# Kernel tuning notes

Measured on AMD Instinct MI355X. Metric: run time of the kernel, lower is better.

The kernel has to match this reference:

```python
import jax, jax.numpy as jnp
import numpy as np
from jax import lax

EPS = 1e-20
_A, _B, _C = slice(None, -2), slice(1, -1), slice(2, None)
# 4 direction pairs: (up-left, down-right), (up, down), (up-right, down-left), (right, left)
_OFFS = [((_A, _A), (_C, _C)), ((_A, _B), (_C, _B)), ((_A, _C), (_C, _A)), ((_B, _C), (_B, _A))]


def _neigh(x, pad_val):
    # x: [B,C,H,W] -> [B,C,9,H,W] of 3x3 neighborhoods (stride 1, pad 1)
    B, C, H, W = x.shape
    xp = jnp.pad(x, ((0, 0), (0, 0), (1, 1), (1, 1)), constant_values=pad_val)
    return jnp.stack([xp[:, :, i:i + H, j:j + W] for i in range(3) for j in range(3)], axis=2)


def _take(n, j):
    return jnp.take_along_axis(n, j, axis=2)[:, :, 0]


def _pair_stack(lo, hi, op):
    # -> [B,C,2,4,H,W]; mirrors the torch stack-of-stacks over 4 directions x 2 orderings
    return jnp.stack([jnp.stack([op(lo[:, :, r1, c1], hi[:, :, r2, c2]),
                                 op(hi[:, :, r1, c1], lo[:, :, r2, c2])], axis=2)
                      for (r1, c1), (r2, c2) in _OFFS], axis=3)


def _forward(d, cd, e, ce, w_prop, w_s_from_d, channel_weight, spatial_weight):
    B, C, H, W = d.shape
    O4 = spatial_weight.shape[0]
    O = O4 // 4
    # pad like F.pad(d, (1,1,1,1))
    dp = jnp.pad(d, ((0, 0), (0, 0), (1, 1), (1, 1)))
    cdp = jnp.pad(cd, ((0, 0), (0, 0), (1, 1), (1, 1)))
    # max_pool2d(k=3,s=1,p=1, return_indices) equivalent: argmax over 3x3 neighborhood,
    # then gather d / cd at those indices (retrieve_indices)
    j_max = jnp.argmax(_neigh(dp * cdp, -np.inf), axis=2, keepdims=True)
    j_min = jnp.argmax(_neigh(cdp / (dp + EPS), -np.inf), axis=2, keepdims=True)
    nd, ncd = _neigh(dp, 0.0), _neigh(cdp, 0.0)
    d_min, d_max = _take(nd, j_min), _take(nd, j_max)
    cd_min, cd_max = _take(ncd, j_min), _take(ncd, j_max)
    # directional depth ratios and confidence products: [B,C,2,4,H,W]
    d_ratio = jnp.clip(_pair_stack(d_min, d_max, lambda a, b: a / (b + EPS)), EPS, 1.0) ** w_s_from_d
    c_ratio = _pair_stack(cd_min, cd_max, lambda a, b: a * b)
    j = jnp.argmax(c_ratio / d_ratio, axis=2, keepdims=True)
    e_from_d = _take(d_ratio, j)   # [B,C,4,H,W]
    ce_from_d = _take(c_ratio, j)  # [B,C,4,H,W]
    # confidence-weighted propagation, then flatten to [B, C*4, H, W]
    e = ((w_prop * ce * e + ce_from_d * e_from_d) / (w_prop * ce + ce_from_d + EPS)).reshape(B, C * 4, H, W)
    ce = ((w_prop * ce + ce_from_d) / (w_prop + 1.0)).reshape(B, C * 4, H, W)
    # 1x1 channel mixing conv (groups=1)
    cw = channel_weight[:, :, 0, 0]  # [O*4, C*4]
    nom = jnp.einsum('bihw,oi->bohw', ce * e, cw)
    den = jnp.einsum('bihw,oi->bohw', ce, cw)
    e = nom / (den + EPS)
    ce = den / (jnp.sum(channel_weight) + EPS)
    # depthwise spatial conv (groups = out*4), stride=1, padding=k//2
    K = spatial_weight.shape[-1]
    p = K // 2
    dw = lambda x: lax.conv_general_dilated(x, spatial_weight, (1, 1), ((p, p), (p, p)),
                                            feature_group_count=O4,
                                            dimension_numbers=('NCHW', 'OIHW', 'NCHW'))
    nom = dw(ce * e).reshape(B, O, 4, H, W)
    den = dw(ce).reshape(B, O, 4, H, W)
    return nom / (den + EPS), den / (jnp.sum(spatial_weight) + EPS)


def setup_inputs() -> dict:
    key = jax.random.key(0)
    ks = jax.random.split(key, 8)
    B, C, O, H, W, K = 4, 32, 32, 192, 192, 5
    d = jax.random.uniform(ks[0], (B, C, H, W), jnp.float32)
    cd = jax.random.uniform(ks[1], (B, C, H, W), jnp.float32)
    e = jax.random.uniform(ks[2], (B, C, 4, H, W), jnp.float32)
    ce = jax.random.uniform(ks[3], (B, C, 4, H, W), jnp.float32)
    # parameters; positive as enforced by enforce_limits() (softplus) in the original
    w_prop = jax.random.uniform(ks[4], (1, C, 1, 1, 1), jnp.float32, 0.5, 1.5)
    w_s_from_d = jax.random.uniform(ks[5], (1, C, 2, 4, 1, 1), jnp.float32, 0.5, 2.0)
    channel_weight = jax.random.uniform(ks[6], (O * 4, C * 4, 1, 1), jnp.float32)
    spatial_weight = jax.random.uniform(ks[7], (O * 4, 1, K, K), jnp.float32)
    return dict(d=d, cd=cd, e=e, ce=ce, w_prop=w_prop, w_s_from_d=w_s_from_d,
                channel_weight=channel_weight, spatial_weight=spatial_weight)


def reference(d, cd, e, ce, w_prop, w_s_from_d, channel_weight, spatial_weight):
    return _forward(d, cd, e, ce, w_prop, w_s_from_d, channel_weight, spatial_weight)
```

## Files before the change

kernel.cpp:

```cpp
#include <hip/hip_runtime.h>
#include <stdint.h>

#define EPS 1e-20f
#define H_ 192
#define W_ 192
#define HW_ 36864
#define CH4 128
#define OUTELEMS 18874368

typedef __attribute__((ext_vector_type(8))) short bf16x8;
typedef __attribute__((ext_vector_type(4))) float f32x4;

__device__ __forceinline__ unsigned short f2bf(float f) {
  unsigned u = __float_as_uint(f);
  return (unsigned short)((u + 0x7fffu + ((u >> 16) & 1u)) >> 16);
}
__device__ __forceinline__ float bflo(unsigned v) { return __uint_as_float(v << 16); }
__device__ __forceinline__ float bfhi(unsigned v) { return __uint_as_float(v & 0xffff0000u); }

__global__ void __launch_bounds__(256) k0_prep(const float* __restrict__ cw,
                                               const float* __restrict__ sw,
                                               unsigned short* __restrict__ AWhi,
                                               unsigned short* __restrict__ AWlo,
                                               float* __restrict__ sums) {
  int tid = threadIdx.x;
  if (blockIdx.x < 64) {
    int n = blockIdx.x * 256 + tid;
    int t = n & 7;
    int l = (n >> 3) & 63;
    int kb = (n >> 9) & 3;
    int ot = n >> 11;
    int o = ot * 16 + (l & 15);
    int i = kb * 32 + (l >> 4) * 8 + t;
    float wv = cw[o * 128 + i];
    unsigned short hi = f2bf(wv);
    float hif = bflo((unsigned)hi);
    unsigned short lo = f2bf(wv - hif);
    AWhi[n] = hi;
    AWlo[n] = lo;
  } else {
    __shared__ float red[256];
    float s = 0.f;
    for (int k = tid; k < 16384; k += 256) s += cw[k];
    red[tid] = s; __syncthreads();
    for (int off = 128; off > 0; off >>= 1) {
      if (tid < off) red[tid] += red[tid + off];
      __syncthreads();
    }
    if (tid == 0) sums[0] = red[0];
    __syncthreads();
    s = 0.f;
    for (int k = tid; k < 3200; k += 256) s += sw[k];
    red[tid] = s; __syncthreads();
    for (int off = 128; off > 0; off >>= 1) {
      if (tid < off) red[tid] += red[tid + off];
      __syncthreads();
    }
    if (tid == 0) sums[1] = red[0];
  }
}

__global__ void __launch_bounds__(256) k1_stage1(
    const float* __restrict__ d, const float* __restrict__ cd,
    const float* __restrict__ e, const float* __restrict__ ce,
    const float* __restrict__ wprop, const float* __restrict__ wsd,
    unsigned* __restrict__ XY) {
  const int tid = threadIdx.x;
  const int tile = blockIdx.x;
  const int th0 = (tile / 6) * 32, tw0 = (tile % 6) * 32;
  const int bc = blockIdx.y;
  const int b = bc >> 5, c = bc & 31;

  __shared__ float S[5184];
  float* dpL = S;
  float* cdpL = S + 1296;
  float* kxL = S + 2592;
  float* knL = S + 3888;

  const float* dB = d + bc * HW_;
  const float* cdB = cd + bc * HW_;
  for (int idx = tid; idx < 1296; idx += 256) {
    int ly = idx / 36, lx = idx % 36;
    int gy = th0 + ly - 2, gx = tw0 + lx - 2;
    float dv = 0.f, cv = 0.f;
    if (gy >= 0 && gy < H_ && gx >= 0 && gx < W_) {
      dv = dB[gy * W_ + gx];
      cv = cdB[gy * W_ + gx];
    }
    dpL[idx] = dv; cdpL[idx] = cv;
    bool inb = (gy >= -1) & (gy <= H_) & (gx >= -1) & (gx <= W_);
    kxL[idx] = inb ? dv * cv : -1.f;
    knL[idx] = inb ? cv / (dv + EPS) : -1.f;
  }
  __syncthreads();

  float rdmn[5], rdmx[5], rcmn[5], rcmx[5];
#pragma unroll
  for (int i = 0; i < 5; ++i) {
    int idx = i * 256 + tid;
    if (idx < 1156) {
      int ly = idx / 34, lx = idx % 34;
      int base = ly * 36 + lx;
      float bkx = -1.f, bkn = -1.f;
      int ox = base + 37, on = base + 37;
#pragma unroll
      for (int di = 0; di < 3; ++di) {
#pragma unroll
        for (int dj = 0; dj < 3; ++dj) {
          int o = base + di * 36 + dj;
          float kx = kxL[o], kn = knL[o];
          if (kx > bkx) { bkx = kx; ox = o; }
          if (kn > bkn) { bkn = kn; on = o; }
        }
      }
      rdmx[i] = dpL[ox]; rcmx[i] = cdpL[ox];
      rdmn[i] = dpL[on]; rcmn[i] = cdpL[on];
    } else {
      rdmx[i] = 0.f; rcmx[i] = 0.f; rdmn[i] = 0.f; rcmn[i] = 0.f;
    }
  }
  __syncthreads();

  float* DMN = S;
  float* DMX = S + 1190;
  float* CMN = S + 2380;
  float* CMX = S + 3570;
#pragma unroll
  for (int i = 0; i < 5; ++i) {
    int idx = i * 256 + tid;
    if (idx < 1156) {
      int ly = idx / 34, lx = idx % 34;
      int m = ly * 35 + lx;
      DMN[m] = rdmn[i]; DMX[m] = rdmx[i];
      CMN[m] = rcmn[i]; CMX[m] = rcmx[i];
    }
  }
  __syncthreads();

  const float wp = wprop[c];
  const float iwp1 = __builtin_amdgcn_rcpf(wp + 1.0f);
  float wq[8];
#pragma unroll
  for (int t = 0; t < 8; ++t) wq[t] = wsd[c * 8 + t];

  const int offy[4] = {-1, -1, -1, 0};
  const int offx[4] = {-1, 0, 1, 1};

  const int ly = tid >> 3, lx4 = (tid & 7) << 2;
  const int hh = th0 + ly, ww0 = tw0 + lx4;
#pragma unroll
  for (int p = 0; p < 4; ++p) {
    int n1 = (ly + offy[p] + 1) * 35 + (lx4 + offx[p] + 1);
    int n2 = (ly - offy[p] + 1) * 35 + (lx4 - offx[p] + 1);
    int ei = (bc * 4 + p) * HW_ + hh * W_ + ww0;
    float4 ev4 = *reinterpret_cast<const float4*>(&e[ei]);
    float4 cev4 = *reinterpret_cast<const float4*>(&ce[ei]);
    const float* evp = &ev4.x;
    const float* cevp = &cev4.x;
    unsigned ow[4];
#pragma unroll
    for (int k = 0; k < 4; ++k) {
      float dmn1 = DMN[n1 + k], cmn1 = CMN[n1 + k];
      float dmx1 = DMX[n1 + k], cmx1 = CMX[n1 + k];
      float dmn2 = DMN[n2 + k], cmn2 = CMN[n2 + k];
      float dmx2 = DMX[n2 + k], cmx2 = CMX[n2 + k];
      float r0 = dmn1 * __builtin_amdgcn_rcpf(dmx2 + EPS);
      float r1 = dmx1 * __builtin_amdgcn_rcpf(dmn2 + EPS);
      float cr0 = cmn1 * cmx2;
      float cr1 = cmx1 * cmn2;
      float x0 = fminf(fmaxf(r0, EPS), 1.0f);
      float x1 = fminf(fmaxf(r1, EPS), 1.0f);
      float dr0 = __builtin_amdgcn_exp2f(wq[p] * __builtin_amdgcn_logf(x0));
      float dr1 = __builtin_amdgcn_exp2f(wq[4 + p] * __builtin_amdgcn_logf(x1));
      float ef, cf;
      if (cr1 * dr0 > cr0 * dr1) { ef = dr1; cf = cr1; } else { ef = dr0; cf = cr0; }
      float ev = evp[k], cev = cevp[k];
      float dn = wp * cev + cf;
      float e1 = (wp * cev * ev + cf * ef) * __builtin_amdgcn_rcpf(dn + EPS);
      float ce1 = dn * iwp1;
      ow[k] = (unsigned)f2bf(ce1 * e1) | ((unsigned)f2bf(ce1) << 16);
    }
    unsigned* xo = &XY[(b * CH4 + c * 4 + p) * HW_ + hh * W_ + ww0];
    *reinterpret_cast<uint4*>(xo) = make_uint4(ow[0], ow[1], ow[2], ow[3]);
  }
}

__global__ void __launch_bounds__(256) k2_mix(const unsigned* __restrict__ XY,
                                              const unsigned short* __restrict__ AWhi,
                                              const unsigned short* __restrict__ AWlo,
                                              const float* __restrict__ sums,
                                              unsigned* __restrict__ PQ) {
  __shared__ unsigned L[128 * 66];
  const int tid = threadIdx.x;
  const int blk = blockIdx.x;
  const int b = blk / 576;
  const int hw0 = (blk % 576) * 64;
  const unsigned* xp = XY + (size_t)(b * CH4) * HW_ + hw0;

#pragma unroll
  for (int j = 0; j < 8; ++j) {
    int v = j * 256 + tid;
    int ch = v >> 4;
    int po = (v & 15) * 4;
    uint4 val = *reinterpret_cast<const uint4*>(xp + (size_t)ch * HW_ + po);
    unsigned* dst = &L[ch * 66 + po];
    *reinterpret_cast<uint2*>(dst) = make_uint2(val.x, val.y);
    *reinterpret_cast<uint2*>(dst + 2) = make_uint2(val.z, val.w);
  }
  __syncthreads();

  const int lane = tid & 63;
  const int w = tid >> 6;
  const int c = lane & 15;
  const int g = lane >> 4;
  const int pbase = w * 16 + c;

  bf16x8 xf[4], yf[4];
#pragma unroll
  for (int kb = 0; kb < 4; ++kb) {
    unsigned vv[8];
    const unsigned* base = &L[(kb * 32 + g * 8) * 66 + pbase];
#pragma unroll
    for (int t = 0; t < 8; ++t) vv[t] = base[t * 66];
    union { bf16x8 v; unsigned u[4]; } ux, uy;
#pragma unroll
    for (int p = 0; p < 4; ++p) {
      ux.u[p] = (vv[2 * p] & 0xffffu) | (vv[2 * p + 1] << 16);
      uy.u[p] = (vv[2 * p] >> 16) | (vv[2 * p + 1] & 0xffff0000u);
    }
    xf[kb] = ux.v;
    yf[kb] = uy.v;
  }

  const float inv = 1.0f / (sums[0] + EPS);
  unsigned* qp = PQ + (size_t)(b * CH4) * HW_ + hw0;

#pragma unroll 2
  for (int ot = 0; ot < 8; ++ot) {
    f32x4 accn = {0.f, 0.f, 0.f, 0.f};
    f32x4 accd = {0.f, 0.f, 0.f, 0.f};
#pragma unroll
    for (int kb = 0; kb < 4; ++kb) {
      int an = ((ot * 4 + kb) * 64 + lane) * 8;
      bf16x8 ahi = *reinterpret_cast<const bf16x8*>(AWhi + an);
      bf16x8 alo = *reinterpret_cast<const bf16x8*>(AWlo + an);
      accn = __builtin_amdgcn_mfma_f32_16x16x32_bf16(ahi, xf[kb], accn, 0, 0, 0);
      accn = __builtin_amdgcn_mfma_f32_16x16x32_bf16(alo, xf[kb], accn, 0, 0, 0);
      accd = __builtin_amdgcn_mfma_f32_16x16x32_bf16(ahi, yf[kb], accd, 0, 0, 0);
      accd = __builtin_amdgcn_mfma_f32_16x16x32_bf16(alo, yf[kb], accd, 0, 0, 0);
    }
#pragma unroll
    for (int j = 0; j < 4; ++j) {
      int o = ot * 16 + g * 4 + j;
      qp[(size_t)o * HW_ + w * 16 + c] =
          (unsigned)f2bf(accn[j] * inv) | ((unsigned)f2bf(accd[j] * inv) << 16);
    }
  }
}

__global__ void __launch_bounds__(256) k3_conv(const unsigned* __restrict__ PQ,
                                               const float* __restrict__ sw,
                                               const float* __restrict__ sums,
                                               float* __restrict__ out0,
                                               float* __restrict__ out1) {
  int t = blockIdx.x;
  int tile = t % 36;
  int chb = t / 36;
  int ch = chb & 127;
  int th0 = (tile / 6) * 32, tw0 = (tile % 6) * 32;
  __shared__ float Pt[1296], Qt[1296];
  const unsigned* src = PQ + chb * HW_;
  int tid = threadIdx.x;
  for (int idx = tid; idx < 1296; idx += 256) {
    int ly = idx / 36, lx = idx % 36;
    int gy = th0 + ly - 2, gx = tw0 + lx - 2;
    unsigned v = 0;
    if (gy >= 0 && gy < H_ && gx >= 0 && gx < W_) v = src[gy * W_ + gx];
    Pt[idx] = bflo(v); Qt[idx] = bfhi(v);
  }
  __syncthreads();
  float wr[25];
#pragma unroll
  for (int k = 0; k < 25; ++k) wr[k] = sw[ch * 25 + k];
  float isw = 1.0f / (sums[1] + EPS);
  int x = tid & 31, yg = tid >> 5;
  float an[4] = {0, 0, 0, 0}, ad[4] = {0, 0, 0, 0};
#pragma unroll
  for (int rr = 0; rr < 8; ++rr) {
    int Lr = yg * 4 + rr;
    float pv[5], qv[5];
#pragma unroll
    for (int c5 = 0; c5 < 5; ++c5) {
      pv[c5] = Pt[Lr * 36 + x + c5];
      qv[c5] = Qt[Lr * 36 + x + c5];
    }
#pragma unroll
    for (int k = 0; k < 4; ++k) {
      int ky = rr - k;
      if (ky >= 0 && ky <= 4) {
#pragma unroll
        for (int c5 = 0; c5 < 5; ++c5) {
          an[k] += pv[c5] * wr[ky * 5 + c5];
          ad[k] += qv[c5] * wr[ky * 5 + c5];
        }
      }
    }
  }
#pragma unroll
  for (int k = 0; k < 4; ++k) {
    int hh = th0 + yg * 4 + k;
    int oi = chb * HW_ + hh * W_ + tw0 + x;
    out0[oi] = an[k] / (ad[k] + EPS);
    out1[oi] = ad[k] * isw;
  }
}

extern "C" void kernel_launch(void* const* d_in, const int* in_sizes, int n_in,
                              void* d_out, int out_size, void* d_ws, size_t ws_size,
                              hipStream_t stream) {
  const float* d = (const float*)d_in[0];
  const float* cd = (const float*)d_in[1];
  const float* e = (const float*)d_in[2];
  const float* ce = (const float*)d_in[3];
  const float* wprop = (const float*)d_in[4];
  const float* wsd = (const float*)d_in[5];
  const float* cw = (const float*)d_in[6];
  const float* sw = (const float*)d_in[7];

  float* wsf = (float*)d_ws;
  float* sums = wsf;
  unsigned short* AWhi = (unsigned short*)(wsf + 64);
  unsigned short* AWlo = AWhi + 16384;
  unsigned* PQ = (unsigned*)(wsf + 64 + 16384);
  float* out0 = (float*)d_out;
  float* out1 = out0 + OUTELEMS;
  unsigned* XY = (unsigned*)(out0 + OUTELEMS);

  hipLaunchKernelGGL(k0_prep, dim3(65), dim3(256), 0, stream, cw, sw, AWhi, AWlo, sums);
  hipLaunchKernelGGL(k1_stage1, dim3(36, 128), dim3(256), 0, stream, d, cd, e, ce,
                     wprop, wsd, XY);
  hipLaunchKernelGGL(k2_mix, dim3(2304), dim3(256), 0, stream, XY, AWhi, AWlo, sums, PQ);
  hipLaunchKernelGGL(k3_conv, dim3(18432), dim3(256), 0, stream, PQ, sw, sums, out0,
                     out1);
}
```

Baseline: 417.5 us.

## Vectorize LDS/global loads across stages and drop LDS staging in mix kernel

```diff
diff --git a/kernel.cpp b/kernel.cpp
--- a/kernel.cpp
+++ b/kernel.cpp
@@ -71,11 +71,10 @@
   const int bc = blockIdx.y;
   const int b = bc >> 5, c = bc & 31;
 
-  __shared__ float S[5184];
-  float* dpL = S;
-  float* cdpL = S + 1296;
-  float* kxL = S + 2592;
-  float* knL = S + 3888;
+  __shared__ float2 S2[2592];
+  float2* K2 = S2;
+  float2* V2 = S2 + 1296;
+  float* S = (float*)S2;
 
   const float* dB = d + bc * HW_;
   const float* cdB = cd + bc * HW_;
@@ -87,10 +86,11 @@
       dv = dB[gy * W_ + gx];
       cv = cdB[gy * W_ + gx];
     }
-    dpL[idx] = dv; cdpL[idx] = cv;
     bool inb = (gy >= -1) & (gy <= H_) & (gx >= -1) & (gx <= W_);
-    kxL[idx] = inb ? dv * cv : -1.f;
-    knL[idx] = inb ? cv / (dv + EPS) : -1.f;
+    float kx = inb ? dv * cv : -1.f;
+    float kn = inb ? cv / (dv + EPS) : -1.f;
+    K2[idx] = make_float2(kx, kn);
+    V2[idx] = make_float2(dv, cv);
   }
   __syncthreads();
 
@@ -108,13 +108,14 @@
 #pragma unroll
         for (int dj = 0; dj < 3; ++dj) {
           int o = base + di * 36 + dj;
-          float kx = kxL[o], kn = knL[o];
-          if (kx > bkx) { bkx = kx; ox = o; }
-          if (kn > bkn) { bkn = kn; on = o; }
+          float2 kk = K2[o];
+          if (kk.x > bkx) { bkx = kk.x; ox = o; }
+          if (kk.y > bkn) { bkn = kk.y; on = o; }
         }
       }
-      rdmx[i] = dpL[ox]; rcmx[i] = cdpL[ox];
-      rdmn[i] = dpL[on]; rcmn[i] = cdpL[on];
+      float2 vx = V2[ox], vn = V2[on];
+      rdmx[i] = vx.x; rcmx[i] = vx.y;
+      rdmn[i] = vn.x; rcmn[i] = vn.y;
     } else {
       rdmx[i] = 0.f; rcmx[i] = 0.f; rdmn[i] = 0.f; rcmn[i] = 0.f;
     }
@@ -148,15 +149,19 @@
 
   const int ly = tid >> 3, lx4 = (tid & 7) << 2;
   const int hh = th0 + ly, ww0 = tw0 + lx4;
+  float4 ev4[4], cev4[4];
+#pragma unroll
+  for (int p = 0; p < 4; ++p) {
+    int ei = (bc * 4 + p) * HW_ + hh * W_ + ww0;
+    ev4[p] = *reinterpret_cast<const float4*>(&e[ei]);
+    cev4[p] = *reinterpret_cast<const float4*>(&ce[ei]);
+  }
 #pragma unroll
   for (int p = 0; p < 4; ++p) {
     int n1 = (ly + offy[p] + 1) * 35 + (lx4 + offx[p] + 1);
     int n2 = (ly - offy[p] + 1) * 35 + (lx4 - offx[p] + 1);
-    int ei = (bc * 4 + p) * HW_ + hh * W_ + ww0;
-    float4 ev4 = *reinterpret_cast<const float4*>(&e[ei]);
-    float4 cev4 = *reinterpret_cast<const float4*>(&ce[ei]);
-    const float* evp = &ev4.x;
-    const float* cevp = &cev4.x;
+    const float* evp = &ev4[p].x;
+    const float* cevp = &cev4[p].x;
     unsigned ow[4];
 #pragma unroll
     for (int k = 0; k < 4; ++k) {
@@ -190,38 +195,24 @@
                                               const unsigned short* __restrict__ AWlo,
                                               const float* __restrict__ sums,
                                               unsigned* __restrict__ PQ) {
-  __shared__ unsigned L[128 * 66];
   const int tid = threadIdx.x;
   const int blk = blockIdx.x;
   const int b = blk / 576;
   const int hw0 = (blk % 576) * 64;
-  const unsigned* xp = XY + (size_t)(b * CH4) * HW_ + hw0;
-
-#pragma unroll
-  for (int j = 0; j < 8; ++j) {
-    int v = j * 256 + tid;
-    int ch = v >> 4;
-    int po = (v & 15) * 4;
-    uint4 val = *reinterpret_cast<const uint4*>(xp + (size_t)ch * HW_ + po);
-    unsigned* dst = &L[ch * 66 + po];
-    *reinterpret_cast<uint2*>(dst) = make_uint2(val.x, val.y);
-    *reinterpret_cast<uint2*>(dst + 2) = make_uint2(val.z, val.w);
-  }
-  __syncthreads();
 
   const int lane = tid & 63;
   const int w = tid >> 6;
   const int c = lane & 15;
   const int g = lane >> 4;
-  const int pbase = w * 16 + c;
+  const int px = hw0 + w * 16 + c;
+  const unsigned* xp = XY + (size_t)(b * CH4) * HW_ + px;
 
   bf16x8 xf[4], yf[4];
 #pragma unroll
   for (int kb = 0; kb < 4; ++kb) {
     unsigned vv[8];
-    const unsigned* base = &L[(kb * 32 + g * 8) * 66 + pbase];
-#pragma unroll
-    for (int t = 0; t < 8; ++t) vv[t] = base[t * 66];
+#pragma unroll
+    for (int t = 0; t < 8; ++t) vv[t] = xp[(size_t)(kb * 32 + g * 8 + t) * HW_];
     union { bf16x8 v; unsigned u[4]; } ux, uy;
 #pragma unroll
     for (int p = 0; p < 4; ++p) {
@@ -233,7 +224,7 @@
   }
 
   const float inv = 1.0f / (sums[0] + EPS);
-  unsigned* qp = PQ + (size_t)(b * CH4) * HW_ + hw0;
+  unsigned* qp = PQ + (size_t)(b * CH4) * HW_ + px;
 
 #pragma unroll 2
   for (int ot = 0; ot < 8; ++ot) {
@@ -252,7 +243,7 @@
 #pragma unroll
     for (int j = 0; j < 4; ++j) {
       int o = ot * 16 + g * 4 + j;
-      qp[(size_t)o * HW_ + w * 16 + c] =
+      qp[(size_t)o * HW_] =
           (unsigned)f2bf(accn[j] * inv) | ((unsigned)f2bf(accd[j] * inv) << 16);
     }
   }
@@ -268,15 +259,21 @@
   int chb = t / 36;
   int ch = chb & 127;
   int th0 = (tile / 6) * 32, tw0 = (tile % 6) * 32;
-  __shared__ float Pt[1296], Qt[1296];
-  const unsigned* src = PQ + chb * HW_;
+  __shared__ float Pt[1440], Qt[1440];
+  const unsigned* src = PQ + (size_t)chb * HW_;
   int tid = threadIdx.x;
-  for (int idx = tid; idx < 1296; idx += 256) {
-    int ly = idx / 36, lx = idx % 36;
-    int gy = th0 + ly - 2, gx = tw0 + lx - 2;
-    unsigned v = 0;
-    if (gy >= 0 && gy < H_ && gx >= 0 && gx < W_) v = src[gy * W_ + gx];
-    Pt[idx] = bflo(v); Qt[idx] = bfhi(v);
+  for (int idx = tid; idx < 360; idx += 256) {
+    int ly = idx / 10, q = idx - ly * 10;
+    int gy = th0 + ly - 2;
+    int gx = tw0 - 4 + q * 4;
+    uint4 v = make_uint4(0, 0, 0, 0);
+    if (gy >= 0 && gy < H_ && gx >= 0 && gx < W_)
+      v = *reinterpret_cast<const uint4*>(src + gy * W_ + gx);
+    float4 pv4, qv4;
+    pv4.x = bflo(v.x); pv4.y = bflo(v.y); pv4.z = bflo(v.z); pv4.w = bflo(v.w);
+    qv4.x = bfhi(v.x); qv4.y = bfhi(v.y); qv4.z = bfhi(v.z); qv4.w = bfhi(v.w);
+    *reinterpret_cast<float4*>(&Pt[ly * 40 + q * 4]) = pv4;
+    *reinterpret_cast<float4*>(&Qt[ly * 40 + q * 4]) = qv4;
   }
   __syncthreads();
   float wr[25];
@@ -291,8 +288,8 @@
     float pv[5], qv[5];
 #pragma unroll
     for (int c5 = 0; c5 < 5; ++c5) {
-      pv[c5] = Pt[Lr * 36 + x + c5];
-      qv[c5] = Qt[Lr * 36 + x + c5];
+      pv[c5] = Pt[Lr * 40 + x + 2 + c5];
+      qv[c5] = Qt[Lr * 40 + x + 2 + c5];
     }
 #pragma unroll
     for (int k = 0; k < 4; ++k) {
```

Result: faster. 407.7 us (-2.3%).
